# Performance work log

Measured on AMD Instinct MI355X. Metric: run time of the kernel, lower is better.

The kernel has to match this reference:

```python
import jax, jax.numpy as jnp
import numpy as np

M, D, S, K, DIN = 512, 10, 16384, 1024, 784  # test points, classes, jacobian dim, n_eigh, input dim


def setup_inputs() -> dict:
    key = jax.random.key(0)
    k0, k1, k2, k3, k4 = jax.random.split(key, 5)
    X_test = jax.random.normal(k0, (M, DIN), dtype=jnp.float32)
    Jz = jax.random.normal(k1, (M, D, S), dtype=jnp.float32) * 0.02      # backend.jacobians(X_test)
    v = jax.random.normal(k2, (S, K), dtype=jnp.float32) * 0.02          # self.v from fit()
    A = jax.random.normal(k3, (K, K), dtype=jnp.float32) * 0.02
    G_inv = 0.5 * (A + A.T) + jnp.eye(K, dtype=jnp.float32)              # symmetric, like an inverse PSD matrix
    W_net = jax.random.normal(k4, (DIN, D), dtype=jnp.float32) * 0.02    # stand-in for self.net
    return {"X_test": X_test, "Jz": Jz, "v": v, "G_inv": G_inv, "W_net": W_net}


def reference(X_test, Jz, v, G_inv, W_net):
    # phi: (d, m, k) -- per-class ELLA features of each test point
    phi = jnp.einsum('mds,sk->dmk', Jz, v)
    # Full (class, class, n, m) covariance tensor, exactly as the torch module computes it
    K_test = jnp.einsum('ank,kg,bmg->abnm', phi, G_inv, phi)
    mean = X_test @ W_net                                # self.net(X_test)
    var = jnp.diagonal(K_test, axis1=-2, axis2=-1)       # (d, d, n) -- discards off-diagonal n,m
    return mean, jnp.transpose(var, (2, 0, 1))           # (n, d, d)
```

## Files before the change

kernel.cpp:

```cpp
#include <hip/hip_runtime.h>
#include <hip/hip_bf16.h>

#define M_PTS 512
#define D_CLS 10
#define S_DIM 16384
#define K_DIM 1024
#define DIN_  784
#define PHI_ELEMS (5120 * 1024)

typedef short  bf16x8  __attribute__((ext_vector_type(8)));
typedef float  f32x4   __attribute__((ext_vector_type(4)));
typedef uint   uintx4  __attribute__((ext_vector_type(4)));
typedef ushort ushort8 __attribute__((ext_vector_type(8)));

__device__ __forceinline__ ushort f2bfu(float f) {
    __bf16 h = (__bf16)f;
    return __builtin_bit_cast(ushort, h);
}
__device__ __forceinline__ float bfu2f(ushort u) {
    uint x = (uint)u << 16;
    return __builtin_bit_cast(float, x);
}
__device__ __forceinline__ uint pkbf(float a, float b) {
    return (uint)f2bfu(a) | ((uint)f2bfu(b) << 16);
}

__global__ __launch_bounds__(64) void mean_kernel(const float* __restrict__ X,
                                                  const float* __restrict__ W,
                                                  float* __restrict__ out) {
    int m = blockIdx.x;
    int lane = threadIdx.x;
    float acc[D_CLS];
#pragma unroll
    for (int d = 0; d < D_CLS; ++d) acc[d] = 0.f;
    for (int i = lane; i < DIN_; i += 64) {
        float x = X[(size_t)m * DIN_ + i];
#pragma unroll
        for (int d = 0; d < D_CLS; ++d) acc[d] += x * W[i * D_CLS + d];
    }
#pragma unroll
    for (int d = 0; d < D_CLS; ++d) {
        float v = acc[d];
        for (int off = 32; off > 0; off >>= 1) v += __shfl_down(v, off);
        if (lane == 0) out[(size_t)m * D_CLS + d] = v;
    }
}

__global__ __launch_bounds__(256) void cvt_a(const float* __restrict__ src,
                                             ushort* __restrict__ dst, int n8) {
    for (int i = blockIdx.x * 256 + threadIdx.x; i < n8; i += gridDim.x * 256) {
        float4 a = reinterpret_cast<const float4*>(src)[2 * i];
        float4 b = reinterpret_cast<const float4*>(src)[2 * i + 1];
        ushort8 o;
        o[0] = f2bfu(a.x); o[1] = f2bfu(a.y); o[2] = f2bfu(a.z); o[3] = f2bfu(a.w);
        o[4] = f2bfu(b.x); o[5] = f2bfu(b.y); o[6] = f2bfu(b.z); o[7] = f2bfu(b.w);
        reinterpret_cast<ushort8*>(dst)[i] = o;
    }
}

__global__ __launch_bounds__(256) void cvt_bt(const float* __restrict__ v,
                                              ushort* __restrict__ bt) {
    __shared__ float tile[64][65];
    const int kt = blockIdx.x;
    const int ct = blockIdx.y;
    const int t  = threadIdx.x;
    const int col4 = t & 15, row = t >> 4;
#pragma unroll
    for (int i = 0; i < 4; ++i) {
        int r = row + 16 * i;
        float4 v4 = *reinterpret_cast<const float4*>(
            v + (size_t)(kt * 64 + r) * K_DIM + ct * 64 + col4 * 4);
        tile[r][col4 * 4 + 0] = v4.x; tile[r][col4 * 4 + 1] = v4.y;
        tile[r][col4 * 4 + 2] = v4.z; tile[r][col4 * 4 + 3] = v4.w;
    }
    __syncthreads();
#pragma unroll
    for (int i = 0; i < 2; ++i) {
        int cid = i * 256 + t;
        int c = cid >> 3, kc = cid & 7;
        ushort8 o;
#pragma unroll
        for (int j = 0; j < 8; ++j) o[j] = f2bfu(tile[kc * 8 + j][c]);
        *reinterpret_cast<ushort8*>(bt + (size_t)(ct * 64 + c) * S_DIM +
                                    kt * 64 + kc * 8) = o;
    }
}

template <int KSP>
__global__ __launch_bounds__(256, 2) void gemm256(const ushort* __restrict__ A,
                                                  const ushort* __restrict__ BT,
                                                  ushort* __restrict__ Cout) {
    __shared__ ushort As[3][8192];
    __shared__ ushort Bs[3][4096];

    const int nwg = 160 * KSP;
    const int lid = blockIdx.x;
    const int swz = (lid & 7) * (nwg >> 3) + (lid >> 3);
    const int kp  = swz / 160;
    const int rem = swz - kp * 160;
    const int bm  = rem >> 3;
    const int bn  = rem & 7;
    const int KSTEPS = 512 / KSP;
    const int kbase  = kp * (S_DIM / KSP);

    const int t  = threadIdx.x;
    const int l  = t & 63;
    const int wm = (t >> 7) & 1;
    const int wn = (t >> 6) & 1;
    const int lr = l & 15;
    const int kq = l >> 4;

    const ushort* Ablk = A  + (size_t)(bm * 256) * S_DIM + kbase;
    const ushort* Bblk = BT + (size_t)(bn * 128) * S_DIM + kbase;

    f32x4 acc[8][4];
#pragma unroll
    for (int i = 0; i < 8; ++i)
#pragma unroll
        for (int j = 0; j < 4; ++j) acc[i][j] = (f32x4)0.f;

#define STAGE256(BUF, S)                                                        \
    { _Pragma("unroll") for (int i = 0; i < 4; ++i) {                           \
        const int cch = i * 256 + t;                                            \
        const int r = cch >> 2, sl = cch & 3;                                   \
        const ushort* gp = Ablk + (size_t)r * S_DIM + (S) * 32 +                \
                           ((sl ^ ((r >> 1) & 3)) << 3);                        \
        ushort* lp = &As[BUF][(i * 256 + (t & 192)) * 8];                       \
        __builtin_amdgcn_global_load_lds(                                       \
            (const __attribute__((address_space(1))) void*)gp,                  \
            (__attribute__((address_space(3))) void*)lp, 16, 0, 0);             \
      }                                                                         \
      _Pragma("unroll") for (int i = 0; i < 2; ++i) {                           \
        const int cch = i * 256 + t;                                            \
        const int r = cch >> 2, sl = cch & 3;                                   \
        const ushort* gp = Bblk + (size_t)r * S_DIM + (S) * 32 +                \
                           ((sl ^ ((r >> 1) & 3)) << 3);                        \
        ushort* lp = &Bs[BUF][(i * 256 + (t & 192)) * 8];                       \
        __builtin_amdgcn_global_load_lds(                                       \
            (const __attribute__((address_space(1))) void*)gp,                  \
            (__attribute__((address_space(3))) void*)lp, 16, 0, 0);             \
      } }

#define COMP256(BUF)                                                            \
    { bf16x8 fa[8], fb[4];                                                      \
      _Pragma("unroll") for (int mi = 0; mi < 8; ++mi) {                        \
        const int r = wm * 128 + mi * 16 + lr;                                  \
        fa[mi] = *reinterpret_cast<const bf16x8*>(                              \
            &As[BUF][(r * 4 + (kq ^ ((r >> 1) & 3))) * 8]);                     \
      }                                                                         \
      _Pragma("unroll") for (int ni = 0; ni < 4; ++ni) {                        \
        const int c = wn * 64 + ni * 16 + lr;                                   \
        fb[ni] = *reinterpret_cast<const bf16x8*>(                              \
            &Bs[BUF][(c * 4 + (kq ^ ((c >> 1) & 3))) * 8]);                     \
      }                                                                         \
      _Pragma("unroll") for (int ni = 0; ni < 4; ++ni)                          \
        _Pragma("unroll") for (int mi = 0; mi < 8; ++mi)                        \
          acc[mi][ni] = __builtin_amdgcn_mfma_f32_16x16x32_bf16(                \
              fa[mi], fb[ni], acc[mi][ni], 0, 0, 0);                            \
    }

    STAGE256(0, 0)
    STAGE256(1, 1)
    asm volatile("s_waitcnt vmcnt(6)" ::: "memory");
    __builtin_amdgcn_s_barrier();
    __builtin_amdgcn_sched_barrier(0);

    for (int s = 0; s < KSTEPS - 2; ++s) {
        const int sb = (s + 2) % 3, cb = s % 3;
        STAGE256(sb, s + 2)
        __builtin_amdgcn_s_setprio(1);
        COMP256(cb)
        __builtin_amdgcn_s_setprio(0);
        __builtin_amdgcn_sched_barrier(0);
        asm volatile("s_waitcnt vmcnt(6)" ::: "memory");
        __builtin_amdgcn_s_barrier();
        __builtin_amdgcn_sched_barrier(0);
    }
    {
        __builtin_amdgcn_s_setprio(1);
        COMP256((KSTEPS - 2) % 3)
        __builtin_amdgcn_s_setprio(0);
        __builtin_amdgcn_sched_barrier(0);
        asm volatile("s_waitcnt vmcnt(0)" ::: "memory");
        __builtin_amdgcn_s_barrier();
        __builtin_amdgcn_sched_barrier(0);
        COMP256((KSTEPS - 1) % 3)
    }

    ushort* C = Cout + (size_t)kp * PHI_ELEMS;
#pragma unroll
    for (int mi = 0; mi < 8; ++mi) {
        int orow = bm * 256 + wm * 128 + mi * 16 + kq * 4;
#pragma unroll
        for (int ni = 0; ni < 4; ++ni) {
            int ocol = bn * 128 + wn * 64 + ni * 16 + lr;
            ushort* cp = C + (size_t)orow * K_DIM + ocol;
#pragma unroll
            for (int rr = 0; rr < 4; ++rr)
                cp[(size_t)rr * K_DIM] = f2bfu(acc[mi][ni][rr]);
        }
    }
#undef STAGE256
#undef COMP256
}

template <int SD, int KSP>
__global__ __launch_bounds__(256, 3) void gemm_bb(const ushort* __restrict__ A,
                                                  const ushort* __restrict__ BT,
                                                  float* __restrict__ Cout) {
    __shared__ ushort As[3][4096];
    __shared__ ushort Bs[3][4096];

    const int nwg = 320 * KSP;
    const int lid = blockIdx.x;
    const int swz = (lid & 7) * (nwg >> 3) + (lid >> 3);
    const int kp  = swz / 320;
    const int rem = swz - kp * 320;
    const int bm  = rem >> 3;
    const int bn  = rem & 7;
    const int KSTEPS = SD / 32 / KSP;
    const int kbase  = kp * (SD / KSP);

    const int t  = threadIdx.x;
    const int l  = t & 63;
    const int wm = (t >> 7) & 1;
    const int wn = (t >> 6) & 1;
    const int lr = l & 15;
    const int kq = l >> 4;

    const ushort* Ablk = A  + (size_t)(bm * 128) * SD + kbase;
    const ushort* Bblk = BT + (size_t)(bn * 128) * SD + kbase;

    f32x4 acc[4][4];
#pragma unroll
    for (int i = 0; i < 4; ++i)
#pragma unroll
        for (int j = 0; j < 4; ++j) acc[i][j] = (f32x4)0.f;

#define GSTAGE(BUF, S, SRC, DST)                                                \
    { _Pragma("unroll") for (int i = 0; i < 2; ++i) {                           \
        const int cch = i * 256 + t;                                            \
        const int r = cch >> 2, sl = cch & 3;                                   \
        const ushort* gp = SRC + (size_t)r * SD + (S) * 32 +                    \
                           ((sl ^ ((r >> 1) & 3)) << 3);                        \
        ushort* lp = &DST[BUF][(i * 256 + (t & 192)) * 8];                      \
        __builtin_amdgcn_global_load_lds(                                       \
            (const __attribute__((address_space(1))) void*)gp,                  \
            (__attribute__((address_space(3))) void*)lp, 16, 0, 0);             \
      } }

#define GCOMPUTE(BUF)                                                           \
    { bf16x8 fa[4], fb[4];                                                      \
      _Pragma("unroll") for (int mi = 0; mi < 4; ++mi) {                        \
        const int r = wm * 64 + mi * 16 + lr;                                   \
        fa[mi] = *reinterpret_cast<const bf16x8*>(                              \
            &As[BUF][(r * 4 + (kq ^ ((r >> 1) & 3))) * 8]);                     \
      }                                                                         \
      _Pragma("unroll") for (int ni = 0; ni < 4; ++ni) {                        \
        const int c = wn * 64 + ni * 16 + lr;                                   \
        fb[ni] = *reinterpret_cast<const bf16x8*>(                              \
            &Bs[BUF][(c * 4 + (kq ^ ((c >> 1) & 3))) * 8]);                     \
      }                                                                         \
      _Pragma("unroll") for (int ni = 0; ni < 4; ++ni)                          \
        _Pragma("unroll") for (int mi = 0; mi < 4; ++mi)                        \
          acc[mi][ni] = __builtin_amdgcn_mfma_f32_16x16x32_bf16(                \
              fa[mi], fb[ni], acc[mi][ni], 0, 0, 0);                            \
    }

    GSTAGE(0, 0, Ablk, As)
    GSTAGE(0, 0, Bblk, Bs)
    GSTAGE(1, 1, Ablk, As)
    GSTAGE(1, 1, Bblk, Bs)
    asm volatile("s_waitcnt vmcnt(4)" ::: "memory");
    __builtin_amdgcn_s_barrier();
    __builtin_amdgcn_sched_barrier(0);

    for (int s = 0; s < KSTEPS - 2; ++s) {
        const int sb = (s + 2) % 3, cb = s % 3;
        GSTAGE(sb, s + 2, Ablk, As)
        GSTAGE(sb, s + 2, Bblk, Bs)
        __builtin_amdgcn_s_setprio(1);
        GCOMPUTE(cb)
        __builtin_amdgcn_s_setprio(0);
        __builtin_amdgcn_sched_barrier(0);
        asm volatile("s_waitcnt vmcnt(4)" ::: "memory");
        __builtin_amdgcn_s_barrier();
        __builtin_amdgcn_sched_barrier(0);
    }
    {
        __builtin_amdgcn_s_setprio(1);
        GCOMPUTE((KSTEPS - 2) % 3)
        __builtin_amdgcn_s_setprio(0);
        __builtin_amdgcn_sched_barrier(0);
        asm volatile("s_waitcnt vmcnt(0)" ::: "memory");
        __builtin_amdgcn_s_barrier();
        __builtin_amdgcn_sched_barrier(0);
        GCOMPUTE((KSTEPS - 1) % 3)
    }

    float* C = Cout + (size_t)kp * PHI_ELEMS;
#pragma unroll
    for (int mi = 0; mi < 4; ++mi) {
        int orow = bm * 128 + wm * 64 + mi * 16 + kq * 4;
#pragma unroll
        for (int ni = 0; ni < 4; ++ni) {
            int ocol = bn * 128 + wn * 64 + ni * 16 + lr;
            float* cp = C + (size_t)orow * K_DIM + ocol;
#pragma unroll
            for (int rr = 0; rr < 4; ++rr) cp[(size_t)rr * K_DIM] = acc[mi][ni][rr];
        }
    }
#undef GSTAGE
#undef GCOMPUTE
}

__global__ __launch_bounds__(256) void phi_reduce8(const ushort* __restrict__ slabs,
                                                   ushort* __restrict__ phib) {
    const int n8 = PHI_ELEMS / 8;
    for (int i = blockIdx.x * 256 + threadIdx.x; i < n8; i += gridDim.x * 256) {
        float s[8] = {0.f, 0.f, 0.f, 0.f, 0.f, 0.f, 0.f, 0.f};
#pragma unroll
        for (int p = 0; p < 8; ++p) {
            ushort8 u = reinterpret_cast<const ushort8*>(
                slabs + (size_t)p * PHI_ELEMS)[i];
#pragma unroll
            for (int j = 0; j < 8; ++j) s[j] += bfu2f(u[j]);
        }
        ushort8 o;
#pragma unroll
        for (int j = 0; j < 8; ++j) o[j] = f2bfu(s[j]);
        reinterpret_cast<ushort8*>(phib)[i] = o;
    }
}

__global__ __launch_bounds__(256) void var_contract_b(const float* __restrict__ T,
                                                      const ushort* __restrict__ P,
                                                      float* __restrict__ out) {
    __shared__ float red[4][56];
    const int n = blockIdx.x, t = threadIdx.x, lane = t & 63, wid = t >> 6;
    const float*  Tn = T + (size_t)n * D_CLS * K_DIM;
    const ushort* Pn = P + (size_t)n * D_CLS * K_DIM;
    float Ta[D_CLS][4], Pb[D_CLS][4];
#pragma unroll
    for (int a = 0; a < D_CLS; ++a)
#pragma unroll
        for (int j = 0; j < 4; ++j) {
            Ta[a][j] = Tn[a * K_DIM + t + 256 * j];
            Pb[a][j] = bfu2f(Pn[a * K_DIM + t + 256 * j]);
        }
    int p = 0;
#pragma unroll
    for (int a = 0; a < D_CLS; ++a)
#pragma unroll
        for (int b = 0; b <= a; ++b, ++p) {
            float s = Ta[a][0] * Pb[b][0] + Ta[a][1] * Pb[b][1]
                    + Ta[a][2] * Pb[b][2] + Ta[a][3] * Pb[b][3];
#pragma unroll
            for (int off = 32; off > 0; off >>= 1) s += __shfl_down(s, off);
            if (lane == 0) red[wid][p] = s;
        }
    __syncthreads();
    if (t < 55) {
        int a = 0;
        while ((a + 1) * (a + 2) / 2 <= t) ++a;
        int b = t - a * (a + 1) / 2;
        float s = red[0][t] + red[1][t] + red[2][t] + red[3][t];
        float* vout = out + M_PTS * D_CLS + (size_t)n * D_CLS * D_CLS;
        vout[a * D_CLS + b] = s;
        vout[b * D_CLS + a] = s;
    }
}

__global__ __launch_bounds__(256) void var_contract(const float* __restrict__ T,
                                                    const float* __restrict__ P,
                                                    float* __restrict__ out) {
    __shared__ float red[4][56];
    const int n = blockIdx.x, t = threadIdx.x, lane = t & 63, wid = t >> 6;
    const float* Tn = T + (size_t)n * D_CLS * K_DIM;
    const float* Pn = P + (size_t)n * D_CLS * K_DIM;
    float Ta[D_CLS][4], Pb[D_CLS][4];
#pragma unroll
    for (int a = 0; a < D_CLS; ++a)
#pragma unroll
        for (int j = 0; j < 4; ++j) {
            Ta[a][j] = Tn[a * K_DIM + t + 256 * j];
            Pb[a][j] = Pn[a * K_DIM + t + 256 * j];
        }
    int p = 0;
#pragma unroll
    for (int a = 0; a < D_CLS; ++a)
#pragma unroll
        for (int b = 0; b <= a; ++b, ++p) {
            float s = Ta[a][0] * Pb[b][0] + Ta[a][1] * Pb[b][1]
                    + Ta[a][2] * Pb[b][2] + Ta[a][3] * Pb[b][3];
#pragma unroll
            for (int off = 32; off > 0; off >>= 1) s += __shfl_down(s, off);
            if (lane == 0) red[wid][p] = s;
        }
    __syncthreads();
    if (t < 55) {
        int a = 0;
        while ((a + 1) * (a + 2) / 2 <= t) ++a;
        int b = t - a * (a + 1) / 2;
        float s = red[0][t] + red[1][t] + red[2][t] + red[3][t];
        float* vout = out + M_PTS * D_CLS + (size_t)n * D_CLS * D_CLS;
        vout[a * D_CLS + b] = s;
        vout[b * D_CLS + a] = s;
    }
}

template <int KSP, bool F32OUT>
__global__ __launch_bounds__(256) void phi_reduce(float* __restrict__ phi,
                                                  ushort* __restrict__ phib) {
    const int n8 = PHI_ELEMS / 8;
    for (int i = blockIdx.x * 256 + threadIdx.x; i < n8; i += gridDim.x * 256) {
        f32x4 s0 = reinterpret_cast<f32x4*>(phi)[2 * i];
        f32x4 s1 = reinterpret_cast<f32x4*>(phi)[2 * i + 1];
#pragma unroll
        for (int p = 1; p < KSP; ++p) {
            s0 += reinterpret_cast<f32x4*>(phi + (size_t)p * PHI_ELEMS)[2 * i];
            s1 += reinterpret_cast<f32x4*>(phi + (size_t)p * PHI_ELEMS)[2 * i + 1];
        }
        if (F32OUT) {
            reinterpret_cast<f32x4*>(phi)[2 * i]     = s0;
            reinterpret_cast<f32x4*>(phi)[2 * i + 1] = s1;
        }
        ushort8 o;
        o[0] = f2bfu(s0[0]); o[1] = f2bfu(s0[1]); o[2] = f2bfu(s0[2]); o[3] = f2bfu(s0[3]);
        o[4] = f2bfu(s1[0]); o[5] = f2bfu(s1[1]); o[6] = f2bfu(s1[2]); o[7] = f2bfu(s1[3]);
        reinterpret_cast<ushort8*>(phib)[i] = o;
    }
}

__global__ __launch_bounds__(256) void var_kernel_valu(const float* __restrict__ phi,
                                                       const float* __restrict__ G,
                                                       float* __restrict__ out) {
    __shared__ float ph[D_CLS][K_DIM];
    __shared__ float red[4][56];
    const int n = blockIdx.x, t = threadIdx.x, lane = t & 63, wid = t >> 6;
    const size_t base = (size_t)n * D_CLS * K_DIM;
    for (int i = t; i < D_CLS * K_DIM / 4; i += 256)
        reinterpret_cast<float4*>(&ph[0][0])[i] =
            reinterpret_cast<const float4*>(phi + base)[i];
    __syncthreads();
    float Tacc[D_CLS][4];
#pragma unroll
    for (int a = 0; a < D_CLS; ++a)
#pragma unroll
        for (int j = 0; j < 4; ++j) Tacc[a][j] = 0.f;
#pragma unroll 4
    for (int k = 0; k < K_DIM; ++k) {
        const float* Grow = G + (size_t)k * K_DIM + t;
        float g0 = Grow[0], g1 = Grow[256], g2 = Grow[512], g3 = Grow[768];
#pragma unroll
        for (int a = 0; a < D_CLS; ++a) {
            float pv = ph[a][k];
            Tacc[a][0] += pv * g0; Tacc[a][1] += pv * g1;
            Tacc[a][2] += pv * g2; Tacc[a][3] += pv * g3;
        }
    }
    float pb[D_CLS][4];
#pragma unroll
    for (int b = 0; b < D_CLS; ++b)
#pragma unroll
        for (int j = 0; j < 4; ++j) pb[b][j] = ph[b][t + 256 * j];
    int p = 0;
#pragma unroll
    for (int a = 0; a < D_CLS; ++a)
#pragma unroll
        for (int b = 0; b <= a; ++b, ++p) {
            float s = Tacc[a][0] * pb[b][0] + Tacc[a][1] * pb[b][1]
                    + Tacc[a][2] * pb[b][2] + Tacc[a][3] * pb[b][3];
#pragma unroll
            for (int off = 32; off > 0; off >>= 1) s += __shfl_down(s, off);
            if (lane == 0) red[wid][p] = s;
        }
    __syncthreads();
    if (t < 55) {
        int a = 0;
        while ((a + 1) * (a + 2) / 2 <= t) ++a;
        int b = t - a * (a + 1) / 2;
        float s = red[0][t] + red[1][t] + red[2][t] + red[3][t];
        float* vout = out + M_PTS * D_CLS + (size_t)n * D_CLS * D_CLS;
        vout[a * D_CLS + b] = s;
        vout[b * D_CLS + a] = s;
    }
}

extern "C" void kernel_launch(void* const* d_in, const int* in_sizes, int n_in,
                              void* d_out, int out_size, void* d_ws, size_t ws_size,
                              hipStream_t stream) {
    const float* X  = (const float*)d_in[0];
    const float* Jz = (const float*)d_in[1];
    const float* v  = (const float*)d_in[2];
    const float* G  = (const float*)d_in[3];
    const float* W  = (const float*)d_in[4];
    float* out = (float*)d_out;
    float* ws  = (float*)d_ws;

    const size_t PB   = (size_t)PHI_ELEMS * 4;
    const size_t PHB  = (size_t)PHI_ELEMS * 2;
    const size_t A_B  = (size_t)5120 * S_DIM * 2;
    const size_t BT_B = (size_t)K_DIM * S_DIM * 2;
    const size_t G_B  = (size_t)K_DIM * K_DIM * 2;
    const size_t NEW_NEED = 8 * PHB + BT_B + G_B + A_B;
    const size_t MID_NEED = 2 * PB + A_B + BT_B + G_B + PHB;

    hipLaunchKernelGGL(mean_kernel, dim3(M_PTS), dim3(64), 0, stream, X, W, out);

    if (ws_size >= NEW_NEED) {
        ushort* slabs = (ushort*)ws;
        ushort* vTb   = slabs + (size_t)8 * PHI_ELEMS;
        ushort* Gb    = vTb + (size_t)K_DIM * S_DIM;
        ushort* Abf   = Gb + (size_t)K_DIM * K_DIM;
        ushort* phib  = Abf;
        float*  T     = (float*)(Abf + (size_t)PHI_ELEMS);

        hipLaunchKernelGGL(cvt_a, dim3(2048), dim3(256), 0, stream,
                           Jz, Abf, 5120 * S_DIM / 8);
        hipLaunchKernelGGL(cvt_bt, dim3(256, 16), dim3(256), 0, stream, v, vTb);
        hipLaunchKernelGGL(cvt_a, dim3(256), dim3(256), 0, stream,
                           G, Gb, K_DIM * K_DIM / 8);
        hipLaunchKernelGGL(gemm256<8>, dim3(1280), dim3(256), 0, stream,
                           Abf, vTb, slabs);
        hipLaunchKernelGGL(phi_reduce8, dim3(1024), dim3(256), 0, stream,
                           slabs, phib);
        hipLaunchKernelGGL((gemm_bb<K_DIM, 1>), dim3(320), dim3(256), 0, stream,
                           phib, Gb, T);
        hipLaunchKernelGGL(var_contract_b, dim3(M_PTS), dim3(256), 0, stream,
                           T, phib, out);
        return;
    }

    if (ws_size >= MID_NEED) {
        float*  phi  = ws;
        float*  T    = ws + (size_t)PHI_ELEMS;
        ushort* Abf  = (ushort*)(T + PHI_ELEMS);
        ushort* vTb  = Abf + (size_t)5120 * S_DIM;
        ushort* Gb   = vTb + (size_t)K_DIM * S_DIM;
        ushort* phib = Gb + (size_t)K_DIM * K_DIM;

        hipLaunchKernelGGL(cvt_a, dim3(2048), dim3(256), 0, stream,
                           Jz, Abf, 5120 * S_DIM / 8);
        hipLaunchKernelGGL(cvt_bt, dim3(256, 16), dim3(256), 0, stream, v, vTb);
        hipLaunchKernelGGL(cvt_a, dim3(256), dim3(256), 0, stream,
                           G, Gb, K_DIM * K_DIM / 8);
        hipLaunchKernelGGL((gemm_bb<S_DIM, 1>), dim3(320), dim3(256), 0, stream,
                           Abf, vTb, phi);
        hipLaunchKernelGGL((phi_reduce<1, false>), dim3(1024), dim3(256), 0,
                           stream, phi, phib);
        hipLaunchKernelGGL((gemm_bb<K_DIM, 1>), dim3(320), dim3(256), 0, stream,
                           phib, Gb, T);
        hipLaunchKernelGGL(var_contract, dim3(M_PTS), dim3(256), 0, stream,
                           T, phi, out);
        return;
    }

    float* phi = ws;
    hipLaunchKernelGGL((gemm_bb<K_DIM, 1>), dim3(320), dim3(256), 0, stream,
                       (const ushort*)Jz, (const ushort*)v, phi);
    hipLaunchKernelGGL(var_kernel_valu, dim3(M_PTS), dim3(256), 0, stream,
                       phi, G, out);
}
```

Measured before the change: 428.1 us.

## Stream B operand directly into registers and shrink GEMM tile to 128x128

```diff
diff --git a/kernel.cpp b/kernel.cpp
--- a/kernel.cpp
+++ b/kernel.cpp
@@ -10,7 +10,6 @@
 
 typedef short  bf16x8  __attribute__((ext_vector_type(8)));
 typedef float  f32x4   __attribute__((ext_vector_type(4)));
-typedef uint   uintx4  __attribute__((ext_vector_type(4)));
 typedef ushort ushort8 __attribute__((ext_vector_type(8)));
 
 __device__ __forceinline__ ushort f2bfu(float f) {
@@ -20,9 +19,6 @@
 __device__ __forceinline__ float bfu2f(ushort u) {
     uint x = (uint)u << 16;
     return __builtin_bit_cast(float, x);
-}
-__device__ __forceinline__ uint pkbf(float a, float b) {
-    return (uint)f2bfu(a) | ((uint)f2bfu(b) << 16);
 }
 
 __global__ __launch_bounds__(64) void mean_kernel(const float* __restrict__ X,
@@ -87,17 +83,16 @@
 }
 
 template <int KSP>
-__global__ __launch_bounds__(256, 2) void gemm256(const ushort* __restrict__ A,
+__global__ __launch_bounds__(256, 3) void gemm_bd(const ushort* __restrict__ A,
                                                   const ushort* __restrict__ BT,
                                                   ushort* __restrict__ Cout) {
-    __shared__ ushort As[3][8192];
-    __shared__ ushort Bs[3][4096];
-
-    const int nwg = 160 * KSP;
+    __shared__ ushort As[3][4096];
+
+    const int nwg = 320 * KSP;
     const int lid = blockIdx.x;
     const int swz = (lid & 7) * (nwg >> 3) + (lid >> 3);
-    const int kp  = swz / 160;
-    const int rem = swz - kp * 160;
+    const int kp  = swz / 320;
+    const int rem = swz - kp * 320;
     const int bm  = rem >> 3;
     const int bn  = rem & 7;
     const int KSTEPS = 512 / KSP;
@@ -110,17 +105,19 @@
     const int lr = l & 15;
     const int kq = l >> 4;
 
-    const ushort* Ablk = A  + (size_t)(bm * 256) * S_DIM + kbase;
-    const ushort* Bblk = BT + (size_t)(bn * 128) * S_DIM + kbase;
-
-    f32x4 acc[8][4];
-#pragma unroll
-    for (int i = 0; i < 8; ++i)
+    const ushort* Ablk  = A + (size_t)(bm * 128) * S_DIM + kbase;
+    const ushort* Blane = BT + (size_t)(bn * 128 + wn * 64 + lr) * S_DIM +
+                          kbase + kq * 8;
+
+    bf16x8 b0[4], b1[4];
+    f32x4 acc[4][4];
+#pragma unroll
+    for (int i = 0; i < 4; ++i)
 #pragma unroll
         for (int j = 0; j < 4; ++j) acc[i][j] = (f32x4)0.f;
 
-#define STAGE256(BUF, S)                                                        \
-    { _Pragma("unroll") for (int i = 0; i < 4; ++i) {                           \
+#define STAGE_A(BUF, S)                                                         \
+    { _Pragma("unroll") for (int i = 0; i < 2; ++i) {                           \
         const int cch = i * 256 + t;                                            \
         const int r = cch >> 2, sl = cch & 3;                                   \
         const ushort* gp = Ablk + (size_t)r * S_DIM + (S) * 32 +                \
@@ -129,68 +126,72 @@
         __builtin_amdgcn_global_load_lds(                                       \
             (const __attribute__((address_space(1))) void*)gp,                  \
             (__attribute__((address_space(3))) void*)lp, 16, 0, 0);             \
-      }                                                                         \
-      _Pragma("unroll") for (int i = 0; i < 2; ++i) {                           \
-        const int cch = i * 256 + t;                                            \
-        const int r = cch >> 2, sl = cch & 3;                                   \
-        const ushort* gp = Bblk + (size_t)r * S_DIM + (S) * 32 +                \
-                           ((sl ^ ((r >> 1) & 3)) << 3);                        \
-        ushort* lp = &Bs[BUF][(i * 256 + (t & 192)) * 8];                       \
-        __builtin_amdgcn_global_load_lds(                                       \
-            (const __attribute__((address_space(1))) void*)gp,                  \
-            (__attribute__((address_space(3))) void*)lp, 16, 0, 0);             \
       } }
 
-#define COMP256(BUF)                                                            \
-    { bf16x8 fa[8], fb[4];                                                      \
-      _Pragma("unroll") for (int mi = 0; mi < 8; ++mi) {                        \
-        const int r = wm * 128 + mi * 16 + lr;                                  \
+#define LOAD_B(RG, S)                                                           \
+    { _Pragma("unroll") for (int ni = 0; ni < 4; ++ni)                          \
+        RG[ni] = *reinterpret_cast<const bf16x8*>(                              \
+            Blane + (size_t)ni * 16 * S_DIM + (size_t)(S) * 32);                \
+    }
+
+#define COMPUTE(BUF, RG)                                                        \
+    { bf16x8 fa[4];                                                             \
+      _Pragma("unroll") for (int mi = 0; mi < 4; ++mi) {                        \
+        const int r = wm * 64 + mi * 16 + lr;                                   \
         fa[mi] = *reinterpret_cast<const bf16x8*>(                              \
             &As[BUF][(r * 4 + (kq ^ ((r >> 1) & 3))) * 8]);                     \
       }                                                                         \
-      _Pragma("unroll") for (int ni = 0; ni < 4; ++ni) {                        \
-        const int c = wn * 64 + ni * 16 + lr;                                   \
-        fb[ni] = *reinterpret_cast<const bf16x8*>(                              \
-            &Bs[BUF][(c * 4 + (kq ^ ((c >> 1) & 3))) * 8]);                     \
-      }                                                                         \
       _Pragma("unroll") for (int ni = 0; ni < 4; ++ni)                          \
-        _Pragma("unroll") for (int mi = 0; mi < 8; ++mi)                        \
+        _Pragma("unroll") for (int mi = 0; mi < 4; ++mi)                        \
           acc[mi][ni] = __builtin_amdgcn_mfma_f32_16x16x32_bf16(                \
-              fa[mi], fb[ni], acc[mi][ni], 0, 0, 0);                            \
-    }
-
-    STAGE256(0, 0)
-    STAGE256(1, 1)
+              fa[mi], RG[ni], acc[mi][ni], 0, 0, 0);                            \
+    }
+
+    STAGE_A(0, 0)
+    STAGE_A(1, 1)
+    LOAD_B(b0, 0)
     asm volatile("s_waitcnt vmcnt(6)" ::: "memory");
     __builtin_amdgcn_s_barrier();
     __builtin_amdgcn_sched_barrier(0);
 
-    for (int s = 0; s < KSTEPS - 2; ++s) {
-        const int sb = (s + 2) % 3, cb = s % 3;
-        STAGE256(sb, s + 2)
+    const int NIT = (KSTEPS - 2) / 2;
+    for (int s2 = 0; s2 < NIT; ++s2) {
+        const int s = 2 * s2;
+        STAGE_A((s + 2) % 3, s + 2)
+        LOAD_B(b1, s + 1)
         __builtin_amdgcn_s_setprio(1);
-        COMP256(cb)
+        COMPUTE(s % 3, b0)
         __builtin_amdgcn_s_setprio(0);
         __builtin_amdgcn_sched_barrier(0);
         asm volatile("s_waitcnt vmcnt(6)" ::: "memory");
         __builtin_amdgcn_s_barrier();
         __builtin_amdgcn_sched_barrier(0);
+        STAGE_A((s + 3) % 3, s + 3)
+        LOAD_B(b0, s + 2)
+        __builtin_amdgcn_s_setprio(1);
+        COMPUTE((s + 1) % 3, b1)
+        __builtin_amdgcn_s_setprio(0);
+        __builtin_amdgcn_sched_barrier(0);
+        asm volatile("s_waitcnt vmcnt(6)" ::: "memory");
+        __builtin_amdgcn_s_barrier();
+        __builtin_amdgcn_sched_barrier(0);
     }
     {
+        LOAD_B(b1, KSTEPS - 1)
         __builtin_amdgcn_s_setprio(1);
-        COMP256((KSTEPS - 2) % 3)
+        COMPUTE((KSTEPS - 2) % 3, b0)
         __builtin_amdgcn_s_setprio(0);
         __builtin_amdgcn_sched_barrier(0);
-        asm volatile("s_waitcnt vmcnt(0)" ::: "memory");
+        asm volatile("s_waitcnt vmcnt(4)" ::: "memory");
         __builtin_amdgcn_s_barrier();
         __builtin_amdgcn_sched_barrier(0);
-        COMP256((KSTEPS - 1) % 3)
+        COMPUTE((KSTEPS - 1) % 3, b1)
     }
 
     ushort* C = Cout + (size_t)kp * PHI_ELEMS;
 #pragma unroll
-    for (int mi = 0; mi < 8; ++mi) {
-        int orow = bm * 256 + wm * 128 + mi * 16 + kq * 4;
+    for (int mi = 0; mi < 4; ++mi) {
+        int orow = bm * 128 + wm * 64 + mi * 16 + kq * 4;
 #pragma unroll
         for (int ni = 0; ni < 4; ++ni) {
             int ocol = bn * 128 + wn * 64 + ni * 16 + lr;
@@ -200,8 +201,9 @@
                 cp[(size_t)rr * K_DIM] = f2bfu(acc[mi][ni][rr]);
         }
     }
-#undef STAGE256
-#undef COMP256
+#undef STAGE_A
+#undef LOAD_B
+#undef COMPUTE
 }
 
 template <int SD, int KSP>
@@ -371,122 +373,6 @@
     }
 }
 
-__global__ __launch_bounds__(256) void var_contract(const float* __restrict__ T,
-                                                    const float* __restrict__ P,
-                                                    float* __restrict__ out) {
-    __shared__ float red[4][56];
-    const int n = blockIdx.x, t = threadIdx.x, lane = t & 63, wid = t >> 6;
-    const float* Tn = T + (size_t)n * D_CLS * K_DIM;
-    const float* Pn = P + (size_t)n * D_CLS * K_DIM;
-    float Ta[D_CLS][4], Pb[D_CLS][4];
-#pragma unroll
-    for (int a = 0; a < D_CLS; ++a)
-#pragma unroll
-        for (int j = 0; j < 4; ++j) {
-            Ta[a][j] = Tn[a * K_DIM + t + 256 * j];
-            Pb[a][j] = Pn[a * K_DIM + t + 256 * j];
-        }
-    int p = 0;
-#pragma unroll
-    for (int a = 0; a < D_CLS; ++a)
-#pragma unroll
-        for (int b = 0; b <= a; ++b, ++p) {
-            float s = Ta[a][0] * Pb[b][0] + Ta[a][1] * Pb[b][1]
-                    + Ta[a][2] * Pb[b][2] + Ta[a][3] * Pb[b][3];
-#pragma unroll
-            for (int off = 32; off > 0; off >>= 1) s += __shfl_down(s, off);
-            if (lane == 0) red[wid][p] = s;
-        }
-    __syncthreads();
-    if (t < 55) {
-        int a = 0;
-        while ((a + 1) * (a + 2) / 2 <= t) ++a;
-        int b = t - a * (a + 1) / 2;
-        float s = red[0][t] + red[1][t] + red[2][t] + red[3][t];
-        float* vout = out + M_PTS * D_CLS + (size_t)n * D_CLS * D_CLS;
-        vout[a * D_CLS + b] = s;
-        vout[b * D_CLS + a] = s;
-    }
-}
-
-template <int KSP, bool F32OUT>
-__global__ __launch_bounds__(256) void phi_reduce(float* __restrict__ phi,
-                                                  ushort* __restrict__ phib) {
-    const int n8 = PHI_ELEMS / 8;
-    for (int i = blockIdx.x * 256 + threadIdx.x; i < n8; i += gridDim.x * 256) {
-        f32x4 s0 = reinterpret_cast<f32x4*>(phi)[2 * i];
-        f32x4 s1 = reinterpret_cast<f32x4*>(phi)[2 * i + 1];
-#pragma unroll
-        for (int p = 1; p < KSP; ++p) {
-            s0 += reinterpret_cast<f32x4*>(phi + (size_t)p * PHI_ELEMS)[2 * i];
-            s1 += reinterpret_cast<f32x4*>(phi + (size_t)p * PHI_ELEMS)[2 * i + 1];
-        }
-        if (F32OUT) {
-            reinterpret_cast<f32x4*>(phi)[2 * i]     = s0;
-            reinterpret_cast<f32x4*>(phi)[2 * i + 1] = s1;
-        }
-        ushort8 o;
-        o[0] = f2bfu(s0[0]); o[1] = f2bfu(s0[1]); o[2] = f2bfu(s0[2]); o[3] = f2bfu(s0[3]);
-        o[4] = f2bfu(s1[0]); o[5] = f2bfu(s1[1]); o[6] = f2bfu(s1[2]); o[7] = f2bfu(s1[3]);
-        reinterpret_cast<ushort8*>(phib)[i] = o;
-    }
-}
-
-__global__ __launch_bounds__(256) void var_kernel_valu(const float* __restrict__ phi,
-                                                       const float* __restrict__ G,
-                                                       float* __restrict__ out) {
-    __shared__ float ph[D_CLS][K_DIM];
-    __shared__ float red[4][56];
-    const int n = blockIdx.x, t = threadIdx.x, lane = t & 63, wid = t >> 6;
-    const size_t base = (size_t)n * D_CLS * K_DIM;
-    for (int i = t; i < D_CLS * K_DIM / 4; i += 256)
-        reinterpret_cast<float4*>(&ph[0][0])[i] =
-            reinterpret_cast<const float4*>(phi + base)[i];
-    __syncthreads();
-    float Tacc[D_CLS][4];
-#pragma unroll
-    for (int a = 0; a < D_CLS; ++a)
-#pragma unroll
-        for (int j = 0; j < 4; ++j) Tacc[a][j] = 0.f;
-#pragma unroll 4
-    for (int k = 0; k < K_DIM; ++k) {
-        const float* Grow = G + (size_t)k * K_DIM + t;
-        float g0 = Grow[0], g1 = Grow[256], g2 = Grow[512], g3 = Grow[768];
-#pragma unroll
-        for (int a = 0; a < D_CLS; ++a) {
-            float pv = ph[a][k];
-            Tacc[a][0] += pv * g0; Tacc[a][1] += pv * g1;
-            Tacc[a][2] += pv * g2; Tacc[a][3] += pv * g3;
-        }
-    }
-    float pb[D_CLS][4];
-#pragma unroll
-    for (int b = 0; b < D_CLS; ++b)
-#pragma unroll
-        for (int j = 0; j < 4; ++j) pb[b][j] = ph[b][t + 256 * j];
-    int p = 0;
-#pragma unroll
-    for (int a = 0; a < D_CLS; ++a)
-#pragma unroll
-        for (int b = 0; b <= a; ++b, ++p) {
-            float s = Tacc[a][0] * pb[b][0] + Tacc[a][1] * pb[b][1]
-                    + Tacc[a][2] * pb[b][2] + Tacc[a][3] * pb[b][3];
-#pragma unroll
-            for (int off = 32; off > 0; off >>= 1) s += __shfl_down(s, off);
-            if (lane == 0) red[wid][p] = s;
-        }
-    __syncthreads();
-    if (t < 55) {
-        int a = 0;
-        while ((a + 1) * (a + 2) / 2 <= t) ++a;
-        int b = t - a * (a + 1) / 2;
-        float s = red[0][t] + red[1][t] + red[2][t] + red[3][t];
-        float* vout = out + M_PTS * D_CLS + (size_t)n * D_CLS * D_CLS;
-        vout[a * D_CLS + b] = s;
-        vout[b * D_CLS + a] = s;
-    }
-}
-
 extern "C" void kernel_launch(void* const* d_in, const int* in_sizes, int n_in,
                               void* d_out, int out_size, void* d_ws, size_t ws_size,
                               hipStream_t stream) {
@@ -498,13 +384,12 @@
     float* out = (float*)d_out;
     float* ws  = (float*)d_ws;
 
-    const size_t PB   = (size_t)PHI_ELEMS * 4;
     const size_t PHB  = (size_t)PHI_ELEMS * 2;
     const size_t A_B  = (size_t)5120 * S_DIM * 2;
     const size_t BT_B = (size_t)K_DIM * S_DIM * 2;
     const size_t G_B  = (size_t)K_DIM * K_DIM * 2;
     const size_t NEW_NEED = 8 * PHB + BT_B + G_B + A_B;
-    const size_t MID_NEED = 2 * PB + A_B + BT_B + G_B + PHB;
+    const size_t MID_NEED = 1 * PHB + BT_B + G_B + A_B;
 
     hipLaunchKernelGGL(mean_kernel, dim3(M_PTS), dim3(64), 0, stream, X, W, out);
 
@@ -521,7 +406,7 @@
         hipLaunchKernelGGL(cvt_bt, dim3(256, 16), dim3(256), 0, stream, v, vTb);
         hipLaunchKernelGGL(cvt_a, dim3(256), dim3(256), 0, stream,
                            G, Gb, K_DIM * K_DIM / 8);
-        hipLaunchKernelGGL(gemm256<8>, dim3(1280), dim3(256), 0, stream,
+        hipLaunchKernelGGL(gemm_bd<8>, dim3(2560), dim3(256), 0, stream,
                            Abf, vTb, slabs);
         hipLaunchKernelGGL(phi_reduce8, dim3(1024), dim3(256), 0, stream,
                            slabs, phib);
@@ -532,33 +417,23 @@
         return;
     }
 
-    if (ws_size >= MID_NEED) {
-        float*  phi  = ws;
-        float*  T    = ws + (size_t)PHI_ELEMS;
-        ushort* Abf  = (ushort*)(T + PHI_ELEMS);
-        ushort* vTb  = Abf + (size_t)5120 * S_DIM;
+    {
+        ushort* phib = (ushort*)ws;
+        ushort* vTb  = phib + (size_t)PHI_ELEMS;
         ushort* Gb   = vTb + (size_t)K_DIM * S_DIM;
-        ushort* phib = Gb + (size_t)K_DIM * K_DIM;
+        ushort* Abf  = Gb + (size_t)K_DIM * K_DIM;
+        float*  T    = (float*)Abf;
 
         hipLaunchKernelGGL(cvt_a, dim3(2048), dim3(256), 0, stream,
                            Jz, Abf, 5120 * S_DIM / 8);
         hipLaunchKernelGGL(cvt_bt, dim3(256, 16), dim3(256), 0, stream, v, vTb);
         hipLaunchKernelGGL(cvt_a, dim3(256), dim3(256), 0, stream,
                            G, Gb, K_DIM * K_DIM / 8);
-        hipLaunchKernelGGL((gemm_bb<S_DIM, 1>), dim3(320), dim3(256), 0, stream,
-                           Abf, vTb, phi);
-        hipLaunchKernelGGL((phi_reduce<1, false>), dim3(1024), dim3(256), 0,
-                           stream, phi, phib);
+        hipLaunchKernelGGL(gemm_bd<1>, dim3(320), dim3(256), 0, stream,
+                           Abf, vTb, phib);
         hipLaunchKernelGGL((gemm_bb<K_DIM, 1>), dim3(320), dim3(256), 0, stream,
                            phib, Gb, T);
-        hipLaunchKernelGGL(var_contract, dim3(M_PTS), dim3(256), 0, stream,
-                           T, phi, out);
-        return;
-    }
-
-    float* phi = ws;
-    hipLaunchKernelGGL((gemm_bb<K_DIM, 1>), dim3(320), dim3(256), 0, stream,
-                       (const ushort*)Jz, (const ushort*)v, phi);
-    hipLaunchKernelGGL(var_kernel_valu, dim3(M_PTS), dim3(256), 0, stream,
-                       phi, G, out);
-}
+        hipLaunchKernelGGL(var_contract_b, dim3(M_PTS), dim3(256), 0, stream,
+                           T, phib, out);
+    }
+}
```

New measurement: 544.2 us. 27.1% more time.
